# Performance work log

Hardware: AMD Instinct MI355X
Metric: run time of the kernel (lower is better)

Reference implementation:

```python
import jax, jax.numpy as jnp
import numpy as np

NUM_HEADS = 12


def setup_inputs() -> dict:
    key = jax.random.key(0)
    ks = jax.random.split(key, 6)
    B, N0, C = 4, 2048, 768
    s = 0.02
    return {
        "x": jax.random.normal(ks[0], (B, N0, C), jnp.float32),
        "w_qkv_diff": jax.random.normal(ks[1], (C, 3 * C), jnp.float32) * s,
        "w_qkv_cond": jax.random.normal(ks[2], (C, 3 * C), jnp.float32) * s,
        "w_proj_diff": jax.random.normal(ks[3], (C, C), jnp.float32) * s,
        "b_proj_diff": jnp.zeros((C,), jnp.float32),
        "w_proj_cond": jax.random.normal(ks[4], (C, C), jnp.float32) * s,
        "b_proj_cond": jnp.zeros((C,), jnp.float32),
    }


def reference(x, w_qkv_diff, w_qkv_cond, w_proj_diff, b_proj_diff, w_proj_cond, b_proj_cond):
    B, N0, C = x.shape
    H = NUM_HEADS
    hd = C // H
    scale = hd ** -0.5
    N = N0 // 2
    x_diff, x_cond = x[:, :N, :], x[:, N:, :]

    def qkv(xp, w):
        t = (xp @ w).reshape(B, N, 3, H, hd).transpose(2, 0, 3, 1, 4)  # [3,B,H,N,hd]
        return t[0], t[1], t[2]

    q_d, k_d, v_d = qkv(x_diff, w_qkv_diff)
    q_c, k_c, v_c = qkv(x_cond, w_qkv_cond)

    attn_diff = jax.nn.softmax(jnp.einsum('bhnd,bhmd->bhnm', q_d, k_d) * scale, axis=-1)
    attn_cond = jax.nn.softmax(jnp.einsum('bhnd,bhmd->bhnm', q_c, k_c) * scale, axis=-1)

    # diff branch: attn_diff @ v_diff -> proj_diff -> reused with attn_cond
    o_d = jnp.einsum('bhnm,bhmd->bhnd', attn_diff, v_d).transpose(0, 2, 1, 3).reshape(B, N, C)
    o_d = o_d @ w_proj_diff + b_proj_diff
    o_d = o_d.reshape(B, N, H, hd).transpose(0, 2, 1, 3)  # back to [B,H,N,hd]
    o_d = jnp.einsum('bhnm,bhmd->bhnd', attn_cond, o_d).transpose(0, 2, 1, 3).reshape(B, N, C)

    # cond branch
    o_c = jnp.einsum('bhnm,bhmd->bhnd', attn_cond, v_c).transpose(0, 2, 1, 3).reshape(B, N, C)
    o_c = o_c @ w_proj_cond + b_proj_cond

    return jnp.concatenate([o_d, o_c], axis=1)
```

## Files before the change

kernel.cpp:

```cpp
#include <hip/hip_runtime.h>
#include <hip/hip_bf16.h>


#define C_DIM 768
#define HEADS 12
#define HD 64
#define NSEQ 1024
#define BATCH 4
#define SZC 3145728

typedef short bf16x8 __attribute__((ext_vector_type(8)));
typedef _Float16 f16x8 __attribute__((ext_vector_type(8)));
typedef float f32x4 __attribute__((ext_vector_type(4)));
typedef unsigned int u32x4v __attribute__((ext_vector_type(4)));

typedef __attribute__((address_space(3))) unsigned int lds_u32_t;
typedef __attribute__((address_space(1))) const unsigned int glb_u32_t;

__device__ __forceinline__ void gl16(const void* g, void* l) {
  __builtin_amdgcn_global_load_lds((glb_u32_t*)g, (lds_u32_t*)l, 16, 0, 0);
}

__device__ __forceinline__ unsigned short f2h(float x) {
  _Float16 h = (_Float16)x;
  return *reinterpret_cast<unsigned short*>(&h);
}

__global__ __launch_bounds__(256) void split_wT4_k(
    const float* __restrict__ w0, const float* __restrict__ w1,
    const float* __restrict__ w2, const float* __restrict__ w3,
    unsigned short* __restrict__ t0, unsigned short* __restrict__ t1,
    unsigned short* __restrict__ t2, unsigned short* __restrict__ t3)
{
  const int z = blockIdx.z;
  const int N = (z < 2) ? 2304 : 768;
  if (blockIdx.x * 32 >= N) return;
  const float* w = (z == 0) ? w0 : (z == 1) ? w1 : (z == 2) ? w2 : w3;
  unsigned short* th = (z == 0) ? t0 : (z == 1) ? t1 : (z == 2) ? t2 : t3;

  __shared__ float T[32][33];
  const int n0 = blockIdx.x * 32, k0 = blockIdx.y * 32;
  const int tx = threadIdx.x, ty = threadIdx.y;
#pragma unroll
  for (int i = 0; i < 4; ++i) {
    int k = ty + i * 8;
    T[k][tx] = w[(size_t)(k0 + k) * N + n0 + tx];
  }
  __syncthreads();
#pragma unroll
  for (int i = 0; i < 4; ++i) {
    int n = ty + i * 8;
    th[(size_t)(n0 + n) * 768 + k0 + tx] = f2h(T[tx][n]);
  }
}

__global__ __launch_bounds__(256) void split_x_k(
    const float* __restrict__ x, unsigned short* __restrict__ xs)
{
  const size_t i = ((size_t)blockIdx.x * 256 + threadIdx.x) * 8;
  float4 f0 = *(const float4*)(x + i);
  float4 f1 = *(const float4*)(x + i + 4);
  float fa[8] = {f0.x, f0.y, f0.z, f0.w, f1.x, f1.y, f1.z, f1.w};
  unsigned short hv[8];
#pragma unroll
  for (int j = 0; j < 8; ++j) hv[j] = f2h(fa[j]);
  *(bf16x8*)(xs + i) = *(bf16x8*)hv;
}

template <int EPI>
__global__ __launch_bounds__(256) void gemm2_k(
    const unsigned short* __restrict__ A,
    const unsigned short* __restrict__ B0, const unsigned short* __restrict__ B1,
    const float* __restrict__ bias,
    unsigned short* __restrict__ ws_split,
    float* __restrict__ outf,
    unsigned short* __restrict__ vt_out)
{
  __shared__ __attribute__((aligned(16))) unsigned short lds[16384];

  const int tid = threadIdx.x;
  const int lane = tid & 63;
  const int wave = tid >> 6;
  const int wr = wave >> 1, wc = wave & 1;
  const int arow = lane & 15, agrp = lane >> 4;

  int bx, by, half;
  if constexpr (EPI == 0) {
    int orig = blockIdx.x + 18 * blockIdx.y + 576 * blockIdx.z;
    int xcd = orig & 7, l = orig >> 3;
    int g = xcd * 6 + (l / 24);
    int r = l % 24;
    int rest = g / 6;
    bx = (g % 6) * 3 + (r % 3);
    by = (rest & 3) * 8 + (r / 3);
    half = rest >> 2;
  } else {
    int flat = blockIdx.x + 6 * blockIdx.y;
    flat = (flat & 7) * 24 + (flat >> 3);
    bx = flat % 6;
    by = flat / 6;
    half = 0;
  }

  const int m0 = by * 128;
  const int b = m0 >> 10, nloc = m0 & 1023;
  const int c0 = bx * 128;
  const unsigned short* __restrict__ Bp = (EPI == 0 && half) ? B1 : B0;
  const size_t Arow = (EPI == 0) ? (size_t)(b * 2048 + half * 1024 + nloc)
                                 : (size_t)m0;

  const int gr = tid >> 2, gc = (tid & 3) ^ ((tid >> 3) & 3);
  const unsigned short* gA = A + (Arow + gr) * 768 + gc * 8;
  const unsigned short* gB = Bp + (size_t)(c0 + gr) * 768 + gc * 8;
  const int wo = wave * 512;

  f32x4 acc[4][4];
#pragma unroll
  for (int i = 0; i < 4; ++i)
#pragma unroll
    for (int j = 0; j < 4; ++j) acc[i][j] = f32x4{0.f, 0.f, 0.f, 0.f};

  auto stage4 = [&](int k0, int bo) {
    gl16(gA + k0, lds + bo + wo);
    gl16(gA + k0 + 64 * 768, lds + bo + wo + 2048);
    gl16(gB + k0, lds + bo + 4096 + wo);
    gl16(gB + k0 + 64 * 768, lds + bo + 4096 + wo + 2048);
  };

  stage4(0, 0);
  asm volatile("s_waitcnt vmcnt(0)" ::: "memory");
  __builtin_amdgcn_s_barrier();

  int cur = 0;
  for (int t = 0; t < 24; ++t) {
    const int bo = cur * 8192;
    if (t < 23) stage4((t + 1) * 32, bo ^ 8192);

    f16x8 af[4], bf[4];
#pragma unroll
    for (int mf = 0; mf < 4; ++mf) {
      const int row = wr * 64 + mf * 16 + arow;
      const int off = bo + row * 32 + ((agrp ^ ((row >> 1) & 3)) << 3);
      af[mf] = *(const f16x8*)(lds + off);
    }
#pragma unroll
    for (int nf = 0; nf < 4; ++nf) {
      const int row = wc * 64 + nf * 16 + arow;
      const int off = bo + row * 32 + ((agrp ^ ((row >> 1) & 3)) << 3);
      bf[nf] = *(const f16x8*)(lds + 4096 + off);
    }
#pragma unroll
    for (int mf = 0; mf < 4; ++mf)
#pragma unroll
      for (int nf = 0; nf < 4; ++nf)
        acc[mf][nf] = __builtin_amdgcn_mfma_f32_16x16x32_f16(af[mf], bf[nf], acc[mf][nf], 0, 0, 0);

    if (t < 23) {
      asm volatile("s_waitcnt vmcnt(0)" ::: "memory");
      __builtin_amdgcn_s_barrier();
      cur ^= 1;
    }
  }

  if constexpr (EPI == 0) {
    const int t_ = c0 / 768;
    const int rem0 = c0 - t_ * 768;
    unsigned short* base = ws_split + (size_t)(half * 3) * SZC;
    const float qs = (t_ == 0) ? 0.125f : 1.0f;
#pragma unroll
    for (int nf = 0; nf < 4; ++nf) {
      const int rc = rem0 + wc * 64 + nf * 16 + arow;
      const int h = rc >> 6;
      const int d = rc & 63;
      const size_t bh_ = (size_t)(b * HEADS + h);
      if (t_ < 2) {
        unsigned short* arr = base + (size_t)t_ * SZC;
#pragma unroll
        for (int mf = 0; mf < 4; ++mf) {
#pragma unroll
          for (int ri = 0; ri < 4; ++ri) {
            const int n = nloc + wr * 64 + mf * 16 + agrp * 4 + ri;
            arr[(bh_ * NSEQ + n) * HD + d] = f2h(acc[mf][nf][ri] * qs);
          }
        }
      } else {
        unsigned short* vt_a = base + 2 * (size_t)SZC;
#pragma unroll
        for (int mf = 0; mf < 4; ++mf) {
          const int n = nloc + wr * 64 + mf * 16 + agrp * 4;
          unsigned short hv[4];
#pragma unroll
          for (int ri = 0; ri < 4; ++ri) hv[ri] = f2h(acc[mf][nf][ri]);
          *(ushort4*)(vt_a + (bh_ * HD + d) * NSEQ + n) = *(ushort4*)hv;
        }
      }
    }
  } else if constexpr (EPI == 1) {
#pragma unroll
    for (int nf = 0; nf < 4; ++nf) {
      const int cg = c0 + wc * 64 + nf * 16 + arow;
      const float bv = bias[cg];
#pragma unroll
      for (int mf = 0; mf < 4; ++mf) {
#pragma unroll
        for (int ri = 0; ri < 4; ++ri) {
          const int m = m0 + wr * 64 + mf * 16 + agrp * 4 + ri;
          const int bb = m >> 10, n = m & 1023;
          outf[(size_t)bb * (2048 * 768) + (size_t)(1024 + n) * 768 + cg] =
              acc[mf][nf][ri] + bv;
        }
      }
    }
  } else {
#pragma unroll
    for (int nf = 0; nf < 4; ++nf) {
      const int cg = c0 + wc * 64 + nf * 16 + arow;
      const int h = cg >> 6, d = cg & 63;
      const float bv = bias[cg];
#pragma unroll
      for (int mf = 0; mf < 4; ++mf) {
        const int m = m0 + wr * 64 + mf * 16 + agrp * 4;
        const int bb = m >> 10, n = m & 1023;
        unsigned short hv[4];
#pragma unroll
        for (int ri = 0; ri < 4; ++ri) hv[ri] = f2h(acc[mf][nf][ri] + bv);
        const size_t idx = ((size_t)(bb * HEADS + h) * HD + d) * NSEQ + n;
        *(ushort4*)(vt_out + idx) = *(ushort4*)hv;
      }
    }
  }
}

__global__ __launch_bounds__(256) void attn_single_k(
    const unsigned short* __restrict__ q_, const unsigned short* __restrict__ kk_,
    const unsigned short* __restrict__ vt_,
    unsigned short* __restrict__ osp)
{
  __shared__ __attribute__((aligned(16))) unsigned char lds[33792];
  unsigned char* const ldsK = lds;
  unsigned char* const ldsV = lds + 8192;

  const int tid  = threadIdx.x;
  const int wave = tid >> 6;
  const int lane = tid & 63;

  int flat = blockIdx.x + 16 * blockIdx.y + 192 * blockIdx.z;
  flat = (flat & 7) * 96 + (flat >> 3);
  const int bxq = flat & 15;
  const int h = (flat >> 4) % 12;
  const int b = flat / 192;
  const int bh = b * HEADS + h;
  const int q0 = bxq * 64 + wave * 16;

  unsigned int* const ldsP = (unsigned int*)(lds + 16384) + wave * (16 * 68);
  const int arow = lane & 15;
  const int agrp = lane >> 4;

  f16x8 q8[2];
  {
    const unsigned short* qp = q_ + ((size_t)bh * NSEQ + q0 + arow) * HD + agrp * 8;
    q8[0] = *(const f16x8*)qp;
    q8[1] = *(const f16x8*)(qp + 32);
  }

  f32x4 acc[4];
#pragma unroll
  for (int i = 0; i < 4; ++i) acc[i] = f32x4{0.f, 0.f, 0.f, 0.f};
  float l_run[4] = {0.f, 0.f, 0.f, 0.f};

  const int sr = tid >> 3, sc = tid & 7;
  const int swzc = ((sc ^ (sr & 7)) << 3);
  const size_t kbase = (size_t)bh * NSEQ * HD;
  const size_t vbase = (size_t)bh * HD * NSEQ;
  const unsigned short* gK = kk_ + kbase + (size_t)sr * 64 + swzc;
  const unsigned short* gV = vt_ + vbase + (size_t)sr * NSEQ + swzc;
  const int ldsw = (wave * 8) * 128;

  for (int j0 = 0; j0 < NSEQ; j0 += 64) {
    __syncthreads();
    gl16(gK + j0 * 64, ldsK + ldsw);
    gl16(gK + j0 * 64 + 2048, ldsK + ldsw + 4096);
    gl16(gV + j0, ldsV + ldsw);
    gl16(gV + j0 + 32 * NSEQ, ldsV + ldsw + 4096);
    __syncthreads();

    f32x4 s[4];
#pragma unroll
    for (int nt = 0; nt < 4; ++nt) s[nt] = f32x4{0.f, 0.f, 0.f, 0.f};
#pragma unroll
    for (int ks = 0; ks < 2; ++ks) {
#pragma unroll
      for (int nt = 0; nt < 4; ++nt) {
        const int krow = nt * 16 + arow;
        const int chunk = ks * 4 + agrp;
        const int off = krow * 128 + (((chunk ^ (krow & 7)) << 4));
        f16x8 kf = *(const f16x8*)(ldsK + off);
        s[nt] = __builtin_amdgcn_mfma_f32_16x16x32_f16(q8[ks], kf, s[nt], 0, 0, 0);
      }
    }

#pragma unroll
    for (int nt = 0; nt < 4; ++nt) {
#pragma unroll
      for (int r = 0; r < 4; ++r) {
        float p = __expf(s[nt][r]);
        l_run[r] += p;
        ldsP[(agrp * 4 + r) * 68 + nt * 16 + arow] = (unsigned int)f2h(p);
      }
    }

#pragma unroll
    for (int kk = 0; kk < 2; ++kk) {
      const unsigned int* prow = ldsP + arow * 68 + kk * 32 + agrp * 8;
      u32x4v w0 = *(const u32x4v*)prow;
      u32x4v w1 = *(const u32x4v*)(prow + 4);
      bf16x8 raw;
#pragma unroll
      for (int i = 0; i < 4; ++i) {
        raw[i]     = (short)(w0[i] & 0xffffu);
        raw[4 + i] = (short)(w1[i] & 0xffffu);
      }
      f16x8 p8 = *reinterpret_cast<f16x8*>(&raw);
#pragma unroll
      for (int nt2 = 0; nt2 < 4; ++nt2) {
        const int vrow = nt2 * 16 + arow;
        const int chunk = kk * 4 + agrp;
        const int off = vrow * 128 + (((chunk ^ (vrow & 7)) << 4));
        f16x8 vf = *(const f16x8*)(ldsV + off);
        acc[nt2] = __builtin_amdgcn_mfma_f32_16x16x32_f16(p8, vf, acc[nt2], 0, 0, 0);
      }
    }
  }

#pragma unroll
  for (int r = 0; r < 4; ++r) {
    float sm = l_run[r];
    sm += __shfl_xor(sm, 1, 64);
    sm += __shfl_xor(sm, 2, 64);
    sm += __shfl_xor(sm, 4, 64);
    sm += __shfl_xor(sm, 8, 64);
    const float inv = 1.f / sm;
    const int n = q0 + agrp * 4 + r;
    const size_t obase = ((size_t)(b * NSEQ + n)) * C_DIM + h * HD + arow;
#pragma unroll
    for (int nt2 = 0; nt2 < 4; ++nt2)
      osp[obase + nt2 * 16] = f2h(acc[nt2][r] * inv);
  }
}

__global__ __launch_bounds__(256) void attn_fused_k(
    const unsigned short* __restrict__ q_, const unsigned short* __restrict__ kk_,
    const unsigned short* __restrict__ vA_, const unsigned short* __restrict__ vB_,
    float* __restrict__ out1,
    unsigned short* __restrict__ osp)
{
  __shared__ __attribute__((aligned(16))) unsigned char lds[41984];
  unsigned char* const ldsK = lds;
  unsigned char* const ldsA = lds + 8192;
  unsigned char* const ldsB = lds + 16384;

  const int tid  = threadIdx.x;
  const int wave = tid >> 6;
  const int lane = tid & 63;

  int flat = blockIdx.x + 16 * blockIdx.y + 192 * blockIdx.z;
  flat = (flat & 7) * 96 + (flat >> 3);
  const int bxq = flat & 15;
  const int h = (flat >> 4) % 12;
  const int b = flat / 192;
  const int bh = b * HEADS + h;
  const int q0 = bxq * 64 + wave * 16;

  unsigned int* const ldsP = (unsigned int*)(lds + 24576) + wave * (16 * 68);
  const int arow = lane & 15;
  const int agrp = lane >> 4;

  f16x8 q8[2];
  {
    const unsigned short* qp = q_ + ((size_t)bh * NSEQ + q0 + arow) * HD + agrp * 8;
    q8[0] = *(const f16x8*)qp;
    q8[1] = *(const f16x8*)(qp + 32);
  }

  f32x4 acc1[4], acc2[4];
#pragma unroll
  for (int i = 0; i < 4; ++i) {
    acc1[i] = f32x4{0.f, 0.f, 0.f, 0.f};
    acc2[i] = f32x4{0.f, 0.f, 0.f, 0.f};
  }
  float l_run[4] = {0.f, 0.f, 0.f, 0.f};

  const int sr = tid >> 3, sc = tid & 7;
  const int swzc = ((sc ^ (sr & 7)) << 3);
  const size_t kbase = (size_t)bh * NSEQ * HD;
  const size_t vbase = (size_t)bh * HD * NSEQ;
  const unsigned short* gK = kk_ + kbase + (size_t)sr * 64 + swzc;
  const unsigned short* gA = vA_ + vbase + (size_t)sr * NSEQ + swzc;
  const unsigned short* gB = vB_ + vbase + (size_t)sr * NSEQ + swzc;
  const int ldsw = (wave * 8) * 128;

  for (int j0 = 0; j0 < NSEQ; j0 += 64) {
    __syncthreads();
    gl16(gK + j0 * 64, ldsK + ldsw);
    gl16(gK + j0 * 64 + 2048, ldsK + ldsw + 4096);
    gl16(gA + j0, ldsA + ldsw);
    gl16(gA + j0 + 32 * NSEQ, ldsA + ldsw + 4096);
    gl16(gB + j0, ldsB + ldsw);
    gl16(gB + j0 + 32 * NSEQ, ldsB + ldsw + 4096);
    __syncthreads();

    f32x4 s[4];
#pragma unroll
    for (int nt = 0; nt < 4; ++nt) s[nt] = f32x4{0.f, 0.f, 0.f, 0.f};
#pragma unroll
    for (int ks = 0; ks < 2; ++ks) {
#pragma unroll
      for (int nt = 0; nt < 4; ++nt) {
        const int krow = nt * 16 + arow;
        const int chunk = ks * 4 + agrp;
        const int off = krow * 128 + (((chunk ^ (krow & 7)) << 4));
        f16x8 kf = *(const f16x8*)(ldsK + off);
        s[nt] = __builtin_amdgcn_mfma_f32_16x16x32_f16(q8[ks], kf, s[nt], 0, 0, 0);
      }
    }

#pragma unroll
    for (int nt = 0; nt < 4; ++nt) {
#pragma unroll
      for (int r = 0; r < 4; ++r) {
        float p = __expf(s[nt][r]);
        l_run[r] += p;
        ldsP[(agrp * 4 + r) * 68 + nt * 16 + arow] = (unsigned int)f2h(p);
      }
    }

#pragma unroll
    for (int kk = 0; kk < 2; ++kk) {
      const unsigned int* prow = ldsP + arow * 68 + kk * 32 + agrp * 8;
      u32x4v w0 = *(const u32x4v*)prow;
      u32x4v w1 = *(const u32x4v*)(prow + 4);
      bf16x8 raw;
#pragma unroll
      for (int i = 0; i < 4; ++i) {
        raw[i]     = (short)(w0[i] & 0xffffu);
        raw[4 + i] = (short)(w1[i] & 0xffffu);
      }
      f16x8 p8 = *reinterpret_cast<f16x8*>(&raw);
#pragma unroll
      for (int nt2 = 0; nt2 < 4; ++nt2) {
        const int vrow = nt2 * 16 + arow;
        const int chunk = kk * 4 + agrp;
        const int off = vrow * 128 + (((chunk ^ (vrow & 7)) << 4));
        f16x8 va = *(const f16x8*)(ldsA + off);
        f16x8 vb = *(const f16x8*)(ldsB + off);
        acc1[nt2] = __builtin_amdgcn_mfma_f32_16x16x32_f16(p8, va, acc1[nt2], 0, 0, 0);
        acc2[nt2] = __builtin_amdgcn_mfma_f32_16x16x32_f16(p8, vb, acc2[nt2], 0, 0, 0);
      }
    }
  }

#pragma unroll
  for (int r = 0; r < 4; ++r) {
    float sm = l_run[r];
    sm += __shfl_xor(sm, 1, 64);
    sm += __shfl_xor(sm, 2, 64);
    sm += __shfl_xor(sm, 4, 64);
    sm += __shfl_xor(sm, 8, 64);
    const float inv = 1.f / sm;
    const int n = q0 + agrp * 4 + r;
    float* rowp = out1 + (size_t)b * (2048 * C_DIM) + (size_t)n * C_DIM + h * HD + arow;
    const size_t obase = ((size_t)(b * NSEQ + n)) * C_DIM + h * HD + arow;
#pragma unroll
    for (int nt2 = 0; nt2 < 4; ++nt2) {
      rowp[nt2 * 16] = acc1[nt2][r] * inv;
      osp[obase + nt2 * 16] = f2h(acc2[nt2][r] * inv);
    }
  }
}

extern "C" void kernel_launch(void* const* d_in, const int* in_sizes, int n_in,
                              void* d_out, int out_size, void* d_ws, size_t ws_size,
                              hipStream_t stream)
{
  const float* x           = (const float*)d_in[0];
  const float* w_qkv_diff  = (const float*)d_in[1];
  const float* w_qkv_cond  = (const float*)d_in[2];
  const float* w_proj_diff = (const float*)d_in[3];
  const float* b_proj_diff = (const float*)d_in[4];
  const float* w_proj_cond = (const float*)d_in[5];
  const float* b_proj_cond = (const float*)d_in[6];
  float* out = (float*)d_out;

  const size_t SZ = SZC;
  const size_t WQ = 2304 * 768;
  const size_t WP = 768 * 768;
  unsigned short* sw = (unsigned short*)d_ws;
  unsigned short* qd  = sw + 0 * SZ;
  unsigned short* kd  = sw + 1 * SZ;
  unsigned short* vtd = sw + 2 * SZ;
  unsigned short* qc  = sw + 3 * SZ;
  unsigned short* kc  = sw + 4 * SZ;
  unsigned short* vtc = sw + 5 * SZ;
  unsigned short* wqdT = sw + 6 * SZ;
  unsigned short* wqcT = wqdT + WQ;
  unsigned short* wpdT = wqcT + WQ;
  unsigned short* wpcT = wpdT + WP;
  unsigned short* osp = wpcT + WP;
  unsigned short* vt2 = qd;
  unsigned short* xs = (unsigned short*)d_out;

  split_wT4_k<<<dim3(72, 24, 4), dim3(32, 8), 0, stream>>>(
      w_qkv_diff, w_qkv_cond, w_proj_diff, w_proj_cond,
      wqdT, wqcT, wpdT, wpcT);
  split_x_k<<<dim3(3072), 256, 0, stream>>>(x, xs);

  gemm2_k<0><<<dim3(18, 32, 2), 256, 0, stream>>>(
      xs, wqdT, wqcT, nullptr, sw, nullptr, nullptr);

  attn_single_k<<<dim3(16, 12, 4), 256, 0, stream>>>(qd, kd, vtd, osp);

  gemm2_k<2><<<dim3(6, 32), 256, 0, stream>>>(
      osp, wpdT, nullptr, b_proj_diff, nullptr, nullptr, vt2);

  attn_fused_k<<<dim3(16, 12, 4), 256, 0, stream>>>(
      qc, kc, vt2, vtc, out, osp);

  gemm2_k<1><<<dim3(6, 32), 256, 0, stream>>>(
      osp, wpcT, nullptr, b_proj_cond, nullptr, out, nullptr);
}
```

Baseline: 166.2 us.

## Triple-buffer GEMM K-loop and transpose MFMA for vectorized Q/K stores

The QKV/projection GEMM kernel moves from double to triple buffering in LDS. It prefetches two K-steps ahead and waits with vmcnt(4) instead of draining all loads, so global loads overlap more with MFMA work. For the Q and K column tiles, the MFMA operands are swapped so each lane holds four consecutive head-dim values, which lets the epilogue write ushort4 stores instead of scattered 16-bit stores. LDS use rises to 48 KB per block, which may reduce occupancy.

```diff
diff --git a/kernel.cpp b/kernel.cpp
--- a/kernel.cpp
+++ b/kernel.cpp
@@ -76,7 +76,7 @@
     float* __restrict__ outf,
     unsigned short* __restrict__ vt_out)
 {
-  __shared__ __attribute__((aligned(16))) unsigned short lds[16384];
+  __shared__ __attribute__((aligned(16))) unsigned short lds[24576];
 
   const int tid = threadIdx.x;
   const int lane = tid & 63;
@@ -108,6 +108,7 @@
   const unsigned short* __restrict__ Bp = (EPI == 0 && half) ? B1 : B0;
   const size_t Arow = (EPI == 0) ? (size_t)(b * 2048 + half * 1024 + nloc)
                                  : (size_t)m0;
+  const bool qk_mode = (EPI == 0) && (bx < 12);
 
   const int gr = tid >> 2, gc = (tid & 3) ^ ((tid >> 3) & 3);
   const unsigned short* gA = A + (Arow + gr) * 768 + gc * 8;
@@ -128,13 +129,17 @@
   };
 
   stage4(0, 0);
-  asm volatile("s_waitcnt vmcnt(0)" ::: "memory");
+  stage4(32, 8192);
+  asm volatile("s_waitcnt vmcnt(4)" ::: "memory");
   __builtin_amdgcn_s_barrier();
 
-  int cur = 0;
+  int bo = 0;
   for (int t = 0; t < 24; ++t) {
-    const int bo = cur * 8192;
-    if (t < 23) stage4((t + 1) * 32, bo ^ 8192);
+    if (t + 2 < 24) {
+      int nbo = bo + 16384;
+      if (nbo >= 24576) nbo -= 24576;
+      stage4((t + 2) * 32, nbo);
+    }
 
     f16x8 af[4], bf[4];
 #pragma unroll
@@ -149,42 +154,61 @@
       const int off = bo + row * 32 + ((agrp ^ ((row >> 1) & 3)) << 3);
       bf[nf] = *(const f16x8*)(lds + 4096 + off);
     }
-#pragma unroll
-    for (int mf = 0; mf < 4; ++mf)
-#pragma unroll
-      for (int nf = 0; nf < 4; ++nf)
-        acc[mf][nf] = __builtin_amdgcn_mfma_f32_16x16x32_f16(af[mf], bf[nf], acc[mf][nf], 0, 0, 0);
-
-    if (t < 23) {
+    if (qk_mode) {
+#pragma unroll
+      for (int mf = 0; mf < 4; ++mf)
+#pragma unroll
+        for (int nf = 0; nf < 4; ++nf)
+          acc[mf][nf] = __builtin_amdgcn_mfma_f32_16x16x32_f16(bf[nf], af[mf], acc[mf][nf], 0, 0, 0);
+    } else {
+#pragma unroll
+      for (int mf = 0; mf < 4; ++mf)
+#pragma unroll
+        for (int nf = 0; nf < 4; ++nf)
+          acc[mf][nf] = __builtin_amdgcn_mfma_f32_16x16x32_f16(af[mf], bf[nf], acc[mf][nf], 0, 0, 0);
+    }
+
+    if (t < 22) {
+      asm volatile("s_waitcnt vmcnt(4)" ::: "memory");
+      __builtin_amdgcn_s_barrier();
+    } else if (t == 22) {
       asm volatile("s_waitcnt vmcnt(0)" ::: "memory");
       __builtin_amdgcn_s_barrier();
-      cur ^= 1;
-    }
+    }
+    bo += 8192;
+    if (bo >= 24576) bo = 0;
   }
 
   if constexpr (EPI == 0) {
     const int t_ = c0 / 768;
     const int rem0 = c0 - t_ * 768;
     unsigned short* base = ws_split + (size_t)(half * 3) * SZC;
-    const float qs = (t_ == 0) ? 0.125f : 1.0f;
-#pragma unroll
-    for (int nf = 0; nf < 4; ++nf) {
-      const int rc = rem0 + wc * 64 + nf * 16 + arow;
-      const int h = rc >> 6;
-      const int d = rc & 63;
-      const size_t bh_ = (size_t)(b * HEADS + h);
-      if (t_ < 2) {
-        unsigned short* arr = base + (size_t)t_ * SZC;
+    if (t_ < 2) {
+      unsigned short* arr = base + (size_t)t_ * SZC;
+      const float qs = (t_ == 0) ? 0.125f : 1.0f;
+#pragma unroll
+      for (int nf = 0; nf < 4; ++nf) {
+        const int rem_c = rem0 + wc * 64 + nf * 16 + agrp * 4;
+        const int h = rem_c >> 6;
+        const int d = rem_c & 63;
+        const size_t bh_ = (size_t)(b * HEADS + h);
 #pragma unroll
         for (int mf = 0; mf < 4; ++mf) {
-#pragma unroll
-          for (int ri = 0; ri < 4; ++ri) {
-            const int n = nloc + wr * 64 + mf * 16 + agrp * 4 + ri;
-            arr[(bh_ * NSEQ + n) * HD + d] = f2h(acc[mf][nf][ri] * qs);
-          }
+          const int n = nloc + wr * 64 + mf * 16 + arow;
+          unsigned short hv[4];
+#pragma unroll
+          for (int ri = 0; ri < 4; ++ri) hv[ri] = f2h(acc[mf][nf][ri] * qs);
+          *(ushort4*)(arr + (bh_ * NSEQ + n) * HD + d) = *(ushort4*)hv;
         }
-      } else {
-        unsigned short* vt_a = base + 2 * (size_t)SZC;
+      }
+    } else {
+      unsigned short* vt_a = base + 2 * (size_t)SZC;
+#pragma unroll
+      for (int nf = 0; nf < 4; ++nf) {
+        const int rc = rem0 + wc * 64 + nf * 16 + arow;
+        const int h = rc >> 6;
+        const int d = rc & 63;
+        const size_t bh_ = (size_t)(b * HEADS + h);
 #pragma unroll
         for (int mf = 0; mf < 4; ++mf) {
           const int n = nloc + wr * 64 + mf * 16 + agrp * 4;
```

Measured after the change: 163.0 us. About the same (-1.9%).
